# Kernel tuning notes

Measured on AMD Instinct MI355X. Metric: run time of the kernel, lower is better.

## Reference

```python
import jax, jax.numpy as jnp
import numpy as np

B, S = 4, 2048
IN, OUT = 4096, 11008  # LLaMA-7B FFN up-proj


def setup_inputs() -> dict:
    key = jax.random.key(0)
    k1, k2, k3, k4 = jax.random.split(key, 4)
    x = jax.random.normal(k1, (B, S, IN), dtype=jnp.float32)
    # int4 quantized weight values in [-8, 7], then nibble-pack pairs into bytes
    q = jax.random.randint(k2, (OUT, IN), -8, 8, dtype=jnp.int32)
    lo = q[:, 0::2] & 15           # even-index element -> low nibble
    hi = q[:, 1::2] & 15           # odd-index element  -> high nibble
    weight_q = (lo | (hi << 4)).astype(jnp.int32)  # packed bytes, values in [0, 255], shape [OUT, IN//2]
    # per-output-channel absmax scale (positive floats)
    scale = jax.random.uniform(k3, (OUT,), minval=0.005, maxval=0.02, dtype=jnp.float32)
    bias = jax.random.normal(k4, (OUT,), dtype=jnp.float32) * 0.01
    return {"x": x, "weight_q": weight_q, "scale": scale, "bias": bias}


def _unpack_int4(packed):
    # packed: [out, in//2] ints holding byte values in [0,255]
    lo = packed & 15
    hi = (packed >> 4) & 15
    # sign-extend 4-bit nibbles: values >= 8 map to value - 16 (range [-8, 7])
    lo = lo - 16 * (lo >= 8)
    hi = hi - 16 * (hi >= 8)
    # interleave: even indices = lo, odd indices = hi -> [out, in]
    return jnp.stack([lo, hi], axis=-1).reshape(packed.shape[0], packed.shape[1] * 2)


def reference(x, weight_q, scale, bias):
    # on-the-fly dequant: w[o, i] = q[o, i] * scale[o]
    w = _unpack_int4(weight_q).astype(x.dtype) * scale.astype(x.dtype)[:, None]  # [OUT, IN]
    # F.linear(x, w, bias) == x @ w.T + bias
    return jnp.einsum('bsi,oi->bso', x, w) + bias.astype(x.dtype)
```

## Files before the change

kernel.cpp:

```cpp
#include <hip/hip_runtime.h>
#include <hip/hip_bf16.h>

typedef __attribute__((ext_vector_type(4))) float  f32x4;
typedef __attribute__((ext_vector_type(8))) short  bf16x8;
typedef __attribute__((ext_vector_type(4))) int    i32x4;

#define M_DIM 8192
#define N_DIM 11008
#define K_DIM 4096
#define KP    2048

#define A_WS_BYTES ((size_t)M_DIM * K_DIM * 2)
#define B_WS_BYTES ((size_t)N_DIM * K_DIM * 2)
#define WS_NEED    (A_WS_BYTES + B_WS_BYTES)

#define BM 256
#define BN 256
#define BK 32
#define NT (K_DIM / BK)
#define NBUF 4
#define TILE_A_BYTES (BM * BK * 2)
#define BUF_BYTES    (2 * TILE_A_BYTES)

__device__ __forceinline__ short f2bf(float f) {
    return __builtin_bit_cast(short, __float2bfloat16(f));
}

__global__ __launch_bounds__(256)
void cvt_x_kernel(const float* __restrict__ x, short* __restrict__ xb)
{
    const size_t i = ((size_t)blockIdx.x * 256 + threadIdx.x) * 8;
    const f32x4 a = *(const f32x4*)(x + i);
    const f32x4 b = *(const f32x4*)(x + i + 4);
    bf16x8 o;
    #pragma unroll
    for (int j = 0; j < 4; ++j) {
        o[j]     = f2bf(a[j]);
        o[4 + j] = f2bf(b[j]);
    }
    *(bf16x8*)(xb + i) = o;
}

__global__ __launch_bounds__(256)
void dequant_w_kernel(const int* __restrict__ wq, short* __restrict__ wb)
{
    const size_t i = ((size_t)blockIdx.x * 256 + threadIdx.x) * 4;
    const i32x4 v = *(const i32x4*)(wq + i);
    bf16x8 o;
    #pragma unroll
    for (int j = 0; j < 4; ++j) {
        const int q = (v[j] & 0xFF) ^ 0x88;
        o[2 * j]     = f2bf((float)((q & 15) - 8));
        o[2 * j + 1] = f2bf((float)(((q >> 4) & 15) - 8));
    }
    *(bf16x8*)(wb + i * 2) = o;
}

__global__ __launch_bounds__(512, 2)
void gemm256_kernel(const short* __restrict__ A,
                    const short* __restrict__ Bw,
                    const float* __restrict__ scale,
                    const float* __restrict__ bias,
                    float* __restrict__ out)
{
    __shared__ char lds[NBUF * BUF_BYTES];

    const int t    = threadIdx.x;
    const int lane = t & 63;
    const int wv   = t >> 6;
    const int wm   = wv >> 2;
    const int wn   = wv & 3;

    const int nbx = N_DIM / BN;
    const int cpx = (nbx * (M_DIM / BM)) >> 3;
    const int bid = blockIdx.x;
    const int sid = (bid & 7) * cpx + (bid >> 3);
    const int by  = sid / nbx;
    const int bx  = sid - by * nbx;
    const int m0  = by * BM;
    const int n0  = bx * BN;

    const int srow = lane >> 2;
    const int gp   = lane & 3;

    const short* aSrc[2];
    const short* bSrc[2];
    int aDst[2], bDst[2];
    #pragma unroll
    for (int i = 0; i < 2; ++i) {
        const int c   = wv * 2 + i;
        const int row = c * 16 + srow;
        const int g   = gp ^ ((row >> 1) & 3);
        aSrc[i] = A  + (size_t)(m0 + row) * K_DIM + g * 8;
        bSrc[i] = Bw + (size_t)(n0 + row) * K_DIM + g * 8;
        aDst[i] = c * 1024;
        bDst[i] = TILE_A_BYTES + c * 1024;
    }

#define STAGE(kt_) do {                                                                   \
    const int b_  = (kt_) & (NBUF - 1);                                                   \
    const int ko_ = (kt_) * BK;                                                           \
    _Pragma("unroll")                                                                     \
    for (int i_ = 0; i_ < 2; ++i_) {                                                      \
        __builtin_amdgcn_global_load_lds(                                                 \
            (const __attribute__((address_space(1))) unsigned int*)(aSrc[i_] + ko_),      \
            (__attribute__((address_space(3))) unsigned int*)(lds + b_ * BUF_BYTES + aDst[i_]), \
            16, 0, 0);                                                                    \
        __builtin_amdgcn_global_load_lds(                                                 \
            (const __attribute__((address_space(1))) unsigned int*)(bSrc[i_] + ko_),      \
            (__attribute__((address_space(3))) unsigned int*)(lds + b_ * BUF_BYTES + bDst[i_]), \
            16, 0, 0);                                                                    \
    }                                                                                     \
} while (0)

    const int lr = lane & 15;
    const int lk = lane >> 4;
    int aRd[8], bRd[4];
    #pragma unroll
    for (int mi = 0; mi < 8; ++mi) {
        const int row = wm * 128 + mi * 16 + lr;
        aRd[mi] = row * 64 + ((lk * 16) ^ (((row >> 1) & 3) << 4));
    }
    #pragma unroll
    for (int ni = 0; ni < 4; ++ni) {
        const int row = wn * 64 + ni * 16 + lr;
        bRd[ni] = TILE_A_BYTES + row * 64 + ((lk * 16) ^ (((row >> 1) & 3) << 4));
    }

    f32x4 acc[8][4];
    #pragma unroll
    for (int mi = 0; mi < 8; ++mi)
        #pragma unroll
        for (int ni = 0; ni < 4; ++ni)
            acc[mi][ni] = (f32x4){0.f, 0.f, 0.f, 0.f};

    STAGE(0); STAGE(1); STAGE(2);
    asm volatile("s_waitcnt vmcnt(8)" ::: "memory");
    __builtin_amdgcn_s_barrier();

    for (int kt = 0; kt < NT; ++kt) {
        const char* buf = lds + (kt & (NBUF - 1)) * BUF_BYTES;
        if (kt + 3 < NT) STAGE(kt + 3);

        bf16x8 af[8], bfr[4];
        #pragma unroll
        for (int mi = 0; mi < 8; ++mi) af[mi] = *(const bf16x8*)(buf + aRd[mi]);
        #pragma unroll
        for (int ni = 0; ni < 4; ++ni) bfr[ni] = *(const bf16x8*)(buf + bRd[ni]);

        __builtin_amdgcn_s_setprio(1);
        #pragma unroll
        for (int mi = 0; mi < 8; ++mi)
            #pragma unroll
            for (int ni = 0; ni < 4; ++ni)
                acc[mi][ni] = __builtin_amdgcn_mfma_f32_16x16x32_bf16(
                    af[mi], bfr[ni], acc[mi][ni], 0, 0, 0);
        __builtin_amdgcn_s_setprio(0);

        if (kt < NT - 3)       asm volatile("s_waitcnt vmcnt(8)" ::: "memory");
        else if (kt == NT - 3) asm volatile("s_waitcnt vmcnt(4)" ::: "memory");
        else if (kt == NT - 2) asm volatile("s_waitcnt vmcnt(0)" ::: "memory");
        if (kt < NT - 1) __builtin_amdgcn_s_barrier();
    }

    #pragma unroll
    for (int ni = 0; ni < 4; ++ni) {
        const int gn = n0 + wn * 64 + ni * 16 + lr;
        const float sc = scale[gn];
        const float bi = bias[gn];
        #pragma unroll
        for (int mi = 0; mi < 8; ++mi) {
            const int gm = m0 + wm * 128 + mi * 16 + lk * 4;
            const f32x4 v = acc[mi][ni];
            #pragma unroll
            for (int r = 0; r < 4; ++r)
                out[(size_t)(gm + r) * N_DIM + gn] = v[r] * sc + bi;
        }
    }
#undef STAGE
}

__device__ __forceinline__ int swz(int row, int kbyte) {
    return row * 128 + (kbyte ^ ((row & 7) << 4));
}

__global__ __launch_bounds__(256, 2)
void qlin_kernel(const float* __restrict__ x,
                 const int*   __restrict__ wq,
                 const float* __restrict__ scale,
                 const float* __restrict__ bias,
                 float* __restrict__ out)
{
    __shared__ short As[128 * 64];
    __shared__ short Bs[128 * 64];

    const int t  = threadIdx.x;
    const int n0 = blockIdx.x * 128;
    const int m0 = blockIdx.y * 128;

    const int sr = t >> 1;
    const int sh = t & 1;

    const float* ag = x  + (size_t)(m0 + sr) * K_DIM + sh * 32;
    const int*   bg = wq + (size_t)(n0 + sr) * KP    + sh * 16;

    const int lane = t & 63;
    const int wv   = t >> 6;
    const int wm   = wv >> 1;
    const int wn   = wv & 1;
    const int lr   = lane & 15;
    const int lk   = lane >> 4;

    f32x4 acc[4][4];
    #pragma unroll
    for (int i = 0; i < 4; ++i)
        #pragma unroll
        for (int j = 0; j < 4; ++j)
            acc[i][j] = (f32x4){0.f, 0.f, 0.f, 0.f};

    f32x4 ar[8];
    i32x4 br[4];

    #pragma unroll
    for (int i = 0; i < 8; ++i) ar[i] = *(const f32x4*)(ag + i * 4);
    #pragma unroll
    for (int i = 0; i < 4; ++i) br[i] = *(const i32x4*)(bg + i * 4);

    for (int kt = 0; kt < 64; ++kt) {
        #pragma unroll
        for (int c = 0; c < 4; ++c) {
            bf16x8 pa;
            #pragma unroll
            for (int j = 0; j < 8; ++j)
                pa[j] = f2bf(ar[c * 2 + (j >> 2)][j & 3]);
            *(bf16x8*)((char*)As + swz(sr, sh * 64 + c * 16)) = pa;

            bf16x8 pb;
            #pragma unroll
            for (int j = 0; j < 4; ++j) {
                const int q = br[c][j] ^ 0x88;
                const float flo = __builtin_bit_cast(float, 0x4B000000 | (q & 15))        - 8388616.0f;
                const float fhi = __builtin_bit_cast(float, 0x4B000000 | ((q >> 4) & 15)) - 8388616.0f;
                pb[2 * j]     = f2bf(flo);
                pb[2 * j + 1] = f2bf(fhi);
            }
            *(bf16x8*)((char*)Bs + swz(sr, sh * 64 + c * 16)) = pb;
        }
        __syncthreads();

        if (kt + 1 < 64) {
            const float* an = ag + (kt + 1) * 64;
            const int*   bn = bg + (kt + 1) * 32;
            #pragma unroll
            for (int i = 0; i < 8; ++i) ar[i] = *(const f32x4*)(an + i * 4);
            #pragma unroll
            for (int i = 0; i < 4; ++i) br[i] = *(const i32x4*)(bn + i * 4);
        }

        #pragma unroll
        for (int ks = 0; ks < 2; ++ks) {
            const int kb = ks * 64 + lk * 16;
            bf16x8 af[4], bfr[4];
            #pragma unroll
            for (int mi = 0; mi < 4; ++mi)
                af[mi] = *(const bf16x8*)((const char*)As + swz(wm * 64 + mi * 16 + lr, kb));
            #pragma unroll
            for (int ni = 0; ni < 4; ++ni)
                bfr[ni] = *(const bf16x8*)((const char*)Bs + swz(wn * 64 + ni * 16 + lr, kb));
            #pragma unroll
            for (int mi = 0; mi < 4; ++mi)
                #pragma unroll
                for (int ni = 0; ni < 4; ++ni)
                    acc[mi][ni] = __builtin_amdgcn_mfma_f32_16x16x32_bf16(
                        af[mi], bfr[ni], acc[mi][ni], 0, 0, 0);
        }
        __syncthreads();
    }

    #pragma unroll
    for (int ni = 0; ni < 4; ++ni) {
        const int gn = n0 + wn * 64 + ni * 16 + lr;
        const float sc = scale[gn];
        const float bi = bias[gn];
        #pragma unroll
        for (int mi = 0; mi < 4; ++mi) {
            const int gm = m0 + wm * 64 + mi * 16 + lk * 4;
            const f32x4 v = acc[mi][ni];
            #pragma unroll
            for (int r2 = 0; r2 < 4; ++r2)
                out[(size_t)(gm + r2) * N_DIM + gn] = v[r2] * sc + bi;
        }
    }
}

extern "C" void kernel_launch(void* const* d_in, const int* in_sizes, int n_in,
                              void* d_out, int out_size, void* d_ws, size_t ws_size,
                              hipStream_t stream)
{
    const float* x     = (const float*)d_in[0];
    const int*   wq    = (const int*)d_in[1];
    const float* scale = (const float*)d_in[2];
    const float* bias  = (const float*)d_in[3];
    float*       out   = (float*)d_out;

    if (ws_size >= WS_NEED) {
        short* xb = (short*)d_ws;
        short* wb = (short*)((char*)d_ws + A_WS_BYTES);
        cvt_x_kernel<<<16384, 256, 0, stream>>>(x, xb);
        dequant_w_kernel<<<22016, 256, 0, stream>>>(wq, wb);
        const int nwg = (N_DIM / BN) * (M_DIM / BM);
        gemm256_kernel<<<nwg, 512, 0, stream>>>(xb, wb, scale, bias, out);
    } else {
        qlin_kernel<<<dim3(N_DIM / 128, M_DIM / 128), 256, 0, stream>>>(x, wq, scale, bias, out);
    }
}
```

Baseline: 810.9 us.

## Split GEMM k-step into two MFMA phases interleaved with staged A/B prefetch

Restructures the main GEMM loop so each K step runs as two half-tiles of MFMAs, issuing the A prefetch before the first half and the B prefetch before the second, with barriers and lgkmcnt waits between phases. The loop is unrolled by four so the LDS buffer index is a compile-time constant. The staging layout moves to a flat per-thread row mapping with a simpler XOR swizzle on the read side. Register pressure should drop because only half the A fragments are live at once, but the extra barriers per step may add sync stalls.

```diff
diff --git a/kernel.cpp b/kernel.cpp
--- a/kernel.cpp
+++ b/kernel.cpp
@@ -18,9 +18,7 @@
 #define BN 256
 #define BK 32
 #define NT (K_DIM / BK)
-#define NBUF 4
-#define TILE_A_BYTES (BM * BK * 2)
-#define BUF_BYTES    (2 * TILE_A_BYTES)
+#define TILE_BYTES 32768
 
 __device__ __forceinline__ short f2bf(float f) {
     return __builtin_bit_cast(short, __float2bfloat16(f));
@@ -63,7 +61,7 @@
                     const float* __restrict__ bias,
                     float* __restrict__ out)
 {
-    __shared__ char lds[NBUF * BUF_BYTES];
+    __shared__ char lds[4 * TILE_BYTES];
 
     const int t    = threadIdx.x;
     const int lane = t & 63;
@@ -80,51 +78,38 @@
     const int m0  = by * BM;
     const int n0  = bx * BN;
 
-    const int srow = lane >> 2;
-    const int gp   = lane & 3;
-
-    const short* aSrc[2];
-    const short* bSrc[2];
-    int aDst[2], bDst[2];
-    #pragma unroll
-    for (int i = 0; i < 2; ++i) {
-        const int c   = wv * 2 + i;
-        const int row = c * 16 + srow;
-        const int g   = gp ^ ((row >> 1) & 3);
-        aSrc[i] = A  + (size_t)(m0 + row) * K_DIM + g * 8;
-        bSrc[i] = Bw + (size_t)(n0 + row) * K_DIM + g * 8;
-        aDst[i] = c * 1024;
-        bDst[i] = TILE_A_BYTES + c * 1024;
-    }
-
-#define STAGE(kt_) do {                                                                   \
-    const int b_  = (kt_) & (NBUF - 1);                                                   \
-    const int ko_ = (kt_) * BK;                                                           \
-    _Pragma("unroll")                                                                     \
-    for (int i_ = 0; i_ < 2; ++i_) {                                                      \
-        __builtin_amdgcn_global_load_lds(                                                 \
-            (const __attribute__((address_space(1))) unsigned int*)(aSrc[i_] + ko_),      \
-            (__attribute__((address_space(3))) unsigned int*)(lds + b_ * BUF_BYTES + aDst[i_]), \
-            16, 0, 0);                                                                    \
-        __builtin_amdgcn_global_load_lds(                                                 \
-            (const __attribute__((address_space(1))) unsigned int*)(bSrc[i_] + ko_),      \
-            (__attribute__((address_space(3))) unsigned int*)(lds + b_ * BUF_BYTES + bDst[i_]), \
-            16, 0, 0);                                                                    \
-    }                                                                                     \
-} while (0)
+    const int srow = t >> 2;
+    const int lg   = (t & 3) ^ (srow & 3);
+    const short* aS0 = A  + (size_t)(m0 + srow)       * K_DIM + lg * 8;
+    const short* aS1 = A  + (size_t)(m0 + 128 + srow) * K_DIM + lg * 8;
+    const short* bS0 = Bw + (size_t)(n0 + srow)       * K_DIM + lg * 8;
+    const short* bS1 = Bw + (size_t)(n0 + 128 + srow) * K_DIM + lg * 8;
+    const int aD = srow * 64 + (t & 3) * 16;
+
+#define GLDS(SRC, DST) __builtin_amdgcn_global_load_lds(                         \
+        (const __attribute__((address_space(1))) unsigned int*)(SRC),            \
+        (__attribute__((address_space(3))) unsigned int*)(lds + (DST)), 16, 0, 0)
+
+#define STG_A(SB, kt_) do { const int ko_ = (kt_) * BK;                          \
+    GLDS(aS0 + ko_, (SB) * TILE_BYTES + aD);                                     \
+    GLDS(aS1 + ko_, (SB) * TILE_BYTES + aD + 8192); } while (0)
+
+#define STG_B(SB, kt_) do { const int ko_ = (kt_) * BK;                          \
+    GLDS(bS0 + ko_, (SB) * TILE_BYTES + 16384 + aD);                             \
+    GLDS(bS1 + ko_, (SB) * TILE_BYTES + 16384 + aD + 8192); } while (0)
 
     const int lr = lane & 15;
     const int lk = lane >> 4;
-    int aRd[8], bRd[4];
+    int aOff[8], bOff[4];
     #pragma unroll
     for (int mi = 0; mi < 8; ++mi) {
         const int row = wm * 128 + mi * 16 + lr;
-        aRd[mi] = row * 64 + ((lk * 16) ^ (((row >> 1) & 3) << 4));
+        aOff[mi] = row * 64 + ((lk ^ (lr & 3)) * 16);
     }
     #pragma unroll
     for (int ni = 0; ni < 4; ++ni) {
         const int row = wn * 64 + ni * 16 + lr;
-        bRd[ni] = TILE_A_BYTES + row * 64 + ((lk * 16) ^ (((row >> 1) & 3) << 4));
+        bOff[ni] = 16384 + row * 64 + ((lk ^ (lr & 3)) * 16);
     }
 
     f32x4 acc[8][4];
@@ -134,33 +119,59 @@
         for (int ni = 0; ni < 4; ++ni)
             acc[mi][ni] = (f32x4){0.f, 0.f, 0.f, 0.f};
 
-    STAGE(0); STAGE(1); STAGE(2);
-    asm volatile("s_waitcnt vmcnt(8)" ::: "memory");
-    __builtin_amdgcn_s_barrier();
-
-    for (int kt = 0; kt < NT; ++kt) {
-        const char* buf = lds + (kt & (NBUF - 1)) * BUF_BYTES;
-        if (kt + 3 < NT) STAGE(kt + 3);
-
-        bf16x8 af[8], bfr[4];
-        #pragma unroll
-        for (int mi = 0; mi < 8; ++mi) af[mi] = *(const bf16x8*)(buf + aRd[mi]);
-        #pragma unroll
-        for (int ni = 0; ni < 4; ++ni) bfr[ni] = *(const bf16x8*)(buf + bRd[ni]);
-
-        __builtin_amdgcn_s_setprio(1);
-        #pragma unroll
-        for (int mi = 0; mi < 8; ++mi)
-            #pragma unroll
-            for (int ni = 0; ni < 4; ++ni)
-                acc[mi][ni] = __builtin_amdgcn_mfma_f32_16x16x32_bf16(
-                    af[mi], bfr[ni], acc[mi][ni], 0, 0, 0);
-        __builtin_amdgcn_s_setprio(0);
-
-        if (kt < NT - 3)       asm volatile("s_waitcnt vmcnt(8)" ::: "memory");
-        else if (kt == NT - 3) asm volatile("s_waitcnt vmcnt(4)" ::: "memory");
-        else if (kt == NT - 2) asm volatile("s_waitcnt vmcnt(0)" ::: "memory");
-        if (kt < NT - 1) __builtin_amdgcn_s_barrier();
+#define BAR   __builtin_amdgcn_s_barrier()
+#define LGKM0 asm volatile("s_waitcnt lgkmcnt(0)" ::: "memory")
+#define VMC(N) asm volatile("s_waitcnt vmcnt(" #N ")" ::: "memory")
+
+    STG_A(0, 0); STG_B(0, 0);
+    STG_A(1, 1); STG_B(1, 1);
+    STG_A(2, 2); STG_B(2, 2);
+    VMC(8);
+    BAR;
+
+    for (int kt0 = 0; kt0 < NT; kt0 += 4) {
+        #pragma unroll
+        for (int u = 0; u < 4; ++u) {
+            const int kt = kt0 + u;
+            const char* buf = lds + u * TILE_BYTES;
+            const int   sb  = (u + 3) & 3;
+            const bool  pre = (kt + 3 < NT);
+            bf16x8 af_[4], bf_[4];
+
+            #pragma unroll
+            for (int m_ = 0; m_ < 4; ++m_) af_[m_] = *(const bf16x8*)(buf + aOff[m_]);
+            #pragma unroll
+            for (int n_ = 0; n_ < 4; ++n_) bf_[n_] = *(const bf16x8*)(buf + bOff[n_]);
+            if (pre) STG_A(sb, kt + 3);
+            BAR; LGKM0;
+            __builtin_amdgcn_s_setprio(1);
+            #pragma unroll
+            for (int m_ = 0; m_ < 4; ++m_)
+                #pragma unroll
+                for (int n_ = 0; n_ < 4; ++n_)
+                    acc[m_][n_] = __builtin_amdgcn_mfma_f32_16x16x32_bf16(
+                        af_[m_], bf_[n_], acc[m_][n_], 0, 0, 0);
+            __builtin_amdgcn_s_setprio(0);
+            BAR;
+
+            #pragma unroll
+            for (int m_ = 0; m_ < 4; ++m_) af_[m_] = *(const bf16x8*)(buf + aOff[4 + m_]);
+            if (pre) STG_B(sb, kt + 3);
+            BAR; LGKM0;
+            __builtin_amdgcn_s_setprio(1);
+            #pragma unroll
+            for (int m_ = 0; m_ < 4; ++m_)
+                #pragma unroll
+                for (int n_ = 0; n_ < 4; ++n_)
+                    acc[4 + m_][n_] = __builtin_amdgcn_mfma_f32_16x16x32_bf16(
+                        af_[m_], bf_[n_], acc[4 + m_][n_], 0, 0, 0);
+            __builtin_amdgcn_s_setprio(0);
+
+            if (kt < NT - 3)       VMC(8);
+            else if (kt == NT - 3) VMC(4);
+            else if (kt == NT - 2) VMC(0);
+            if (kt < NT - 1) BAR;
+        }
     }
 
     #pragma unroll
@@ -177,7 +188,12 @@
                 out[(size_t)(gm + r) * N_DIM + gn] = v[r] * sc + bi;
         }
     }
-#undef STAGE
+#undef GLDS
+#undef STG_A
+#undef STG_B
+#undef BAR
+#undef LGKM0
+#undef VMC
 }
 
 __device__ __forceinline__ int swz(int row, int kbyte) {
@@ -260,19 +276,19 @@
         #pragma unroll
         for (int ks = 0; ks < 2; ++ks) {
             const int kb = ks * 64 + lk * 16;
-            bf16x8 af[4], bfr[4];
+            bf16x8 af2[4], bf2[4];
             #pragma unroll
             for (int mi = 0; mi < 4; ++mi)
-                af[mi] = *(const bf16x8*)((const char*)As + swz(wm * 64 + mi * 16 + lr, kb));
+                af2[mi] = *(const bf16x8*)((const char*)As + swz(wm * 64 + mi * 16 + lr, kb));
             #pragma unroll
             for (int ni = 0; ni < 4; ++ni)
-                bfr[ni] = *(const bf16x8*)((const char*)Bs + swz(wn * 64 + ni * 16 + lr, kb));
+                bf2[ni] = *(const bf16x8*)((const char*)Bs + swz(wn * 64 + ni * 16 + lr, kb));
             #pragma unroll
             for (int mi = 0; mi < 4; ++mi)
                 #pragma unroll
                 for (int ni = 0; ni < 4; ++ni)
                     acc[mi][ni] = __builtin_amdgcn_mfma_f32_16x16x32_bf16(
-                        af[mi], bfr[ni], acc[mi][ni], 0, 0, 0);
+                        af2[mi], bf2[ni], acc[mi][ni], 0, 0, 0);
         }
         __syncthreads();
     }
```

Measured after the change: 841.2 us. 3.7% more time.
